# Kernel tuning notes

Hardware: AMD Instinct MI355X
Metric: run time of the kernel (lower is better)

The kernel has to match this reference:

```python
import jax, jax.numpy as jnp
import numpy as np

D_MODEL, D_K, D_V, N_HEADS, D_FF = 1024, 64, 64, 16, 2736
EPS_NORM = 1e-12   # F.normalize eps
EPS_RMS = 1e-6     # RMSNorm eps


def _rmsnorm(x, g):
    return x * jax.lax.rsqrt(jnp.mean(x * x, axis=-1, keepdims=True) + EPS_RMS) * g


def _l2norm(x):
    n = jnp.sqrt(jnp.sum(x * x, axis=-1, keepdims=True))
    return x / jnp.maximum(n, EPS_NORM)


def setup_inputs() -> dict:
    key = jax.random.key(0)
    ks = jax.random.split(key, 10)
    B, T = 2, 1024
    s_in = 0.1 / np.sqrt(D_MODEL)   # xavier-like small init, gain 0.1
    s_ff = 0.1 / np.sqrt(D_FF)
    return {
        "x": jax.random.normal(ks[0], (B, T, D_MODEL), jnp.float32),
        "Wq": jax.random.normal(ks[1], (D_MODEL, N_HEADS * D_K), jnp.float32) * s_in,
        "Wk": jax.random.normal(ks[2], (D_MODEL, N_HEADS * D_K), jnp.float32) * s_in,
        "Wv": jax.random.normal(ks[3], (D_MODEL, N_HEADS * D_V), jnp.float32) * s_in,
        "Wg": jax.random.normal(ks[4], (D_MODEL, N_HEADS * D_K), jnp.float32) * s_in,
        "Wo": jax.random.normal(ks[5], (N_HEADS * D_V, D_MODEL), jnp.float32) * s_in,
        "w1": jax.random.normal(ks[6], (D_MODEL, D_FF), jnp.float32) * s_in,
        "w2": jax.random.normal(ks[7], (D_MODEL, D_FF), jnp.float32) * s_in,
        "w3": jax.random.normal(ks[8], (D_FF, D_MODEL), jnp.float32) * s_ff,
        "g_attn": jnp.ones((D_MODEL,), jnp.float32),
        "g_ffn": jnp.ones((D_MODEL,), jnp.float32),
    }


def _gla(h, Wq, Wk, Wv, Wg, Wo):
    B, T, _ = h.shape
    q = _l2norm((h @ Wq).reshape(B, T, N_HEADS, D_K))
    k = _l2norm((h @ Wk).reshape(B, T, N_HEADS, D_K))
    v = (h @ Wv).reshape(B, T, N_HEADS, D_V)
    alpha = jax.nn.sigmoid(h @ Wg).reshape(B, T, N_HEADS, D_K)

    def step(S, inp):
        a_t, k_t, v_t, q_t = inp                       # [B,H,dk],[B,H,dk],[B,H,dv],[B,H,dk]
        S = a_t[..., None] * S + k_t[..., None] * v_t[..., None, :]   # [B,H,dk,dv]
        o_t = jnp.einsum('bhkv,bhk->bhv', S, q_t)
        return S, o_t

    S0 = jnp.zeros((B, N_HEADS, D_K, D_V), h.dtype)
    xs = (jnp.swapaxes(alpha, 0, 1), jnp.swapaxes(k, 0, 1),
          jnp.swapaxes(v, 0, 1), jnp.swapaxes(q, 0, 1))  # time-major [T,B,H,*]
    _, o = jax.lax.scan(step, S0, xs)                    # o: [T,B,H,dv]
    o = jnp.swapaxes(o, 0, 1).reshape(B, T, N_HEADS * D_V)
    return o @ Wo


def reference(x, Wq, Wk, Wv, Wg, Wo, w1, w2, w3, g_attn, g_ffn):
    # Pre-LN GLA block: x -> Norm -> GLA -> +res -> Norm -> SwiGLU -> +res
    h = _rmsnorm(x, g_attn)
    x = x + _gla(h, Wq, Wk, Wv, Wg, Wo)
    h = _rmsnorm(x, g_ffn)
    ffn = (jax.nn.silu(h @ w1) * (h @ w2)) @ w3
    return x + ffn
```

## Files before the change

### kernel.cpp

```cpp
#include <hip/hip_runtime.h>

typedef unsigned short ushort_t;
typedef unsigned int uint32;
typedef short short8 __attribute__((ext_vector_type(8)));
typedef float f32x4 __attribute__((ext_vector_type(4)));

#define MROWS 2048
#define DMODEL 1024
#define NH 16
#define DFF 2736
#define DFFP 2752
#define NBH 32

__device__ __forceinline__ float b2f(ushort_t u) {
  return __builtin_bit_cast(float, ((uint32)u) << 16);
}
__device__ __forceinline__ ushort_t f2b(float f) {
  uint32 u = __builtin_bit_cast(uint32, f);
  return (ushort_t)((u + 0x7FFFu + ((u >> 16) & 1u)) >> 16);
}
__device__ __forceinline__ float san(float v) {
  uint32 u = __builtin_bit_cast(uint32, v);
  return (((u >> 23) & 0xFFu) == 0xFFu) ? 0.0f : v;
}
__device__ __forceinline__ float sclamp(float v, float lim) {
  return fminf(fmaxf(san(v), -lim), lim);
}

typedef const __attribute__((address_space(1))) unsigned int* gas_ptr;
typedef __attribute__((address_space(3))) unsigned int* las_ptr;
__device__ __forceinline__ void gl_lds16(const void* g, void* l) {
  __builtin_amdgcn_global_load_lds((gas_ptr)g, (las_ptr)l, 16, 0, 0);
}

__device__ __forceinline__ void rmsnorm_body(
    const float* __restrict__ x, const float* __restrict__ g,
    ushort_t* __restrict__ out, int row, int tid) {
  size_t base = (size_t)row * DMODEL;
  int c0 = tid * 4;
  float4 t = *(const float4*)(x + base + c0);
  float v[4] = {t.x, t.y, t.z, t.w};
  float s = v[0]*v[0] + v[1]*v[1] + v[2]*v[2] + v[3]*v[3];
  for (int off = 32; off > 0; off >>= 1) s += __shfl_xor(s, off);
  __shared__ float red[4];
  int wave = tid >> 6, lane = tid & 63;
  if (lane == 0) red[wave] = s;
  __syncthreads();
  if (tid == 0) {
    float tt = red[0] + red[1] + red[2] + red[3];
    red[0] = rsqrtf(tt * (1.0f / DMODEL) + 1e-6f);
  }
  __syncthreads();
  float sc = red[0];
  float4 gg = *(const float4*)(g + c0);
  float gv[4] = {gg.x, gg.y, gg.z, gg.w};
  for (int j = 0; j < 4; ++j)
    out[base + c0 + j] = f2b(sclamp(v[j] * sc * gv[j], 1e4f));
}

__global__ __launch_bounds__(256) void rmsnorm_kernel(
    const float* __restrict__ x, const float* __restrict__ g,
    ushort_t* __restrict__ out) {
  rmsnorm_body(x, g, out, blockIdx.x, threadIdx.x);
}

__device__ __forceinline__ void transpose_tile(
    const float* __restrict__ src, ushort_t* __restrict__ d,
    int K, int N, int Kpad, int n0, int k0, int tid) {
  __shared__ ushort_t tile[32][33];
  int tx = tid & 31, ty = tid >> 5;
  #pragma unroll
  for (int i = 0; i < 4; ++i) {
    int k = k0 + ty + i * 8, n = n0 + tx;
    float v = (k < K && n < N) ? src[(size_t)k * N + n] : 0.0f;
    tile[ty + i * 8][tx] = f2b(v);
  }
  __syncthreads();
  #pragma unroll
  for (int i = 0; i < 4; ++i) {
    int r = ty + i * 8;
    d[(size_t)(n0 + r) * Kpad + k0 + tx] = tile[tx][r];
  }
}

__global__ __launch_bounds__(256) void transpose_kernel(
    const float* __restrict__ S0, const float* __restrict__ S1,
    const float* __restrict__ S2, const float* __restrict__ S3,
    ushort_t* __restrict__ dst, int K, int N, int Kpad, int Npad) {
  const float* src = (blockIdx.z == 0) ? S0 : (blockIdx.z == 1) ? S1
                   : (blockIdx.z == 2) ? S2 : S3;
  ushort_t* d = dst + (size_t)blockIdx.z * Npad * Kpad;
  transpose_tile(src, d, K, N, Kpad, blockIdx.x * 32, blockIdx.y * 32,
                 threadIdx.x);
}

__global__ __launch_bounds__(256) void transpose5_kernel(
    const float* __restrict__ S0, const float* __restrict__ S1,
    const float* __restrict__ S2, const float* __restrict__ S3,
    const float* __restrict__ S4,
    ushort_t* __restrict__ dA, ushort_t* __restrict__ dB) {
  int z = blockIdx.z;
  const float* src = (z == 0) ? S0 : (z == 1) ? S1 : (z == 2) ? S2
                   : (z == 3) ? S3 : S4;
  ushort_t* d = (z < 4) ? (dA + (size_t)z * 1024 * 1024) : dB;
  transpose_tile(src, d, 1024, 1024, 1024, blockIdx.x * 32, blockIdx.y * 32,
                 threadIdx.x);
}

__global__ __launch_bounds__(256) void transpose_ffn_kernel(
    const float* __restrict__ w1, const float* __restrict__ w2,
    const float* __restrict__ w3,
    ushort_t* __restrict__ dW12, ushort_t* __restrict__ dW3) {
  int z = blockIdx.z;
  const float* src; ushort_t* d; int K, N, Kpad, Npad;
  if (z < 2) {
    src = z ? w2 : w1; d = dW12 + (size_t)z * DFFP * 1024;
    K = 1024; N = DFF; Kpad = 1024; Npad = DFFP;
  } else {
    src = w3; d = dW3;
    K = DFF; N = 1024; Kpad = DFFP; Npad = 1024;
  }
  int n0 = blockIdx.x * 32, k0 = blockIdx.y * 32;
  if (n0 >= Npad || k0 >= Kpad) return;
  transpose_tile(src, d, K, N, Kpad, n0, k0, threadIdx.x);
}

__global__ __launch_bounds__(256) void setup_kernel(
    const float* __restrict__ x, const float* __restrict__ gat,
    ushort_t* __restrict__ h1,
    const float* __restrict__ Wq, const float* __restrict__ Wk,
    const float* __restrict__ Wv, const float* __restrict__ Wg,
    const float* __restrict__ Wo,
    ushort_t* __restrict__ dQKVG, ushort_t* __restrict__ dWo,
    const float* __restrict__ w1, const float* __restrict__ w2,
    const float* __restrict__ w3,
    ushort_t* __restrict__ dW12, ushort_t* __restrict__ dW3) {
  int bid = blockIdx.x, tid = threadIdx.x;
  if (bid < 2048) {
    rmsnorm_body(x, gat, h1, bid, tid);
  } else if (bid < 7168) {
    int idx = bid - 2048;
    int z = idx >> 10, rem = idx & 1023;
    const float* src = (z == 0) ? Wq : (z == 1) ? Wk : (z == 2) ? Wv
                     : (z == 3) ? Wg : Wo;
    ushort_t* d = (z < 4) ? (dQKVG + (size_t)z * 1024 * 1024) : dWo;
    transpose_tile(src, d, 1024, 1024, 1024, (rem & 31) * 32, (rem >> 5) * 32,
                   tid);
  } else {
    int fidx = bid - 7168;
    const float* src; ushort_t* d; int K, N, Kpad, bx, by;
    if (fidx < 5504) {
      int z = fidx / 2752, t = fidx % 2752;
      src = z ? w2 : w1; d = dW12 + (size_t)z * DFFP * 1024;
      K = 1024; N = DFF; Kpad = 1024;
      bx = t % 86; by = t / 86;
    } else {
      int t2 = fidx - 5504;
      src = w3; d = dW3;
      K = DFF; N = 1024; Kpad = DFFP;
      bx = t2 % 32; by = t2 / 32;
    }
    transpose_tile(src, d, K, N, Kpad, bx * 32, by * 32, tid);
  }
}

template<int MODE, int BM, int BN, int NB, int MINB>
__global__ __launch_bounds__(256, MINB) void gemm_kernel(
    const ushort_t* __restrict__ A, int lda,
    const ushort_t* __restrict__ Bt, int ldb, size_t boff, int K,
    float* __restrict__ outf, ushort_t* __restrict__ outb, int ldc,
    const float* __restrict__ resf) {
  constexpr int WM = BM / 2, WN = BN / 2;
  constexpr int MF = WM / 16, FN = WN / 16;
  __shared__ __align__(16) ushort_t As0[BM * 64];
  __shared__ __align__(16) ushort_t As1[BM * 64];
  __shared__ __align__(16) ushort_t Bs0[NB][BN * 64];
  __shared__ __align__(16) ushort_t Bs1[NB][BN * 64];
  int tid = threadIdx.x;
  int wave = tid >> 6, lane = tid & 63;
  int nwg = gridDim.x * gridDim.y;
  int orig = blockIdx.y * gridDim.x + blockIdx.x;
  int swz = (orig & 7) * (nwg >> 3) + (orig >> 3);
  int n0 = (swz / gridDim.y) * BN, m0 = (swz % gridDim.y) * BM;
  int wm = (wave >> 1) * WM, wn = (wave & 1) * WN;
  int arow = lane >> 3;
  int scol = (((lane & 7) ^ arow) & 7) * 8;
  int fm = lane & 15, fk = (lane >> 4) * 8;
  int xsw = (fm & 7) * 8;
  f32x4 zero = {0.f, 0.f, 0.f, 0.f};
  f32x4 acc[MF][FN];
  f32x4 acc2[NB == 2 ? MF : 1][NB == 2 ? FN : 1];
  #pragma unroll
  for (int i = 0; i < MF; ++i)
    #pragma unroll
    for (int j = 0; j < FN; ++j) {
      acc[i][j] = zero;
      if (NB == 2) acc2[i][j] = zero;
    }
  int nK = K >> 6;
  auto stage = [&](ushort_t (&Ad)[BM * 64], ushort_t (&Bd)[NB][BN * 64],
                   int kt) {
    int k0 = kt << 6;
    #pragma unroll
    for (int i = 0; i < BM / 32; ++i) {
      int g = i * 4 + wave;
      gl_lds16(A + (size_t)(m0 + g * 8 + arow) * lda + k0 + scol, &Ad[g * 512]);
    }
    #pragma unroll
    for (int nb = 0; nb < NB; ++nb)
      #pragma unroll
      for (int i = 0; i < BN / 32; ++i) {
        int g = i * 4 + wave;
        gl_lds16(Bt + nb * boff + (size_t)(n0 + g * 8 + arow) * ldb + k0 + scol,
                 &Bd[nb][g * 512]);
      }
  };
  auto compute = [&](const ushort_t (&Ad)[BM * 64],
                     const ushort_t (&Bd)[NB][BN * 64]) {
    #pragma unroll
    for (int kk = 0; kk < 64; kk += 32) {
      short8 a[MF];
      #pragma unroll
      for (int fi = 0; fi < MF; ++fi)
        a[fi] = *(const short8*)
            &Ad[(wm + fi * 16 + fm) * 64 + ((kk + fk) ^ xsw)];
      #pragma unroll
      for (int fj = 0; fj < FN; ++fj) {
        short8 b = *(const short8*)
            &Bd[0][(wn + fj * 16 + fm) * 64 + ((kk + fk) ^ xsw)];
        #pragma unroll
        for (int fi = 0; fi < MF; ++fi)
          acc[fi][fj] =
              __builtin_amdgcn_mfma_f32_16x16x32_bf16(a[fi], b, acc[fi][fj], 0, 0, 0);
        if (NB == 2) {
          short8 b2 = *(const short8*)
              &Bd[1][(wn + fj * 16 + fm) * 64 + ((kk + fk) ^ xsw)];
          #pragma unroll
          for (int fi = 0; fi < MF; ++fi)
            acc2[fi][fj] =
                __builtin_amdgcn_mfma_f32_16x16x32_bf16(a[fi], b2, acc2[fi][fj], 0, 0, 0);
        }
      }
    }
  };
  stage(As0, Bs0, 0);
  __syncthreads();
  int t = 0;
  for (;;) {
    if (t + 1 < nK) stage(As1, Bs1, t + 1);
    compute(As0, Bs0);
    __syncthreads();
    if (++t == nK) break;
    if (t + 1 < nK) stage(As0, Bs0, t + 1);
    compute(As1, Bs1);
    __syncthreads();
    if (++t == nK) break;
  }
  int rbase = m0 + wm + ((lane >> 4) << 2);
  #pragma unroll
  for (int fi = 0; fi < MF; ++fi)
    #pragma unroll
    for (int fj = 0; fj < FN; ++fj) {
      int col = n0 + wn + fj * 16 + fm;
      #pragma unroll
      for (int reg = 0; reg < 4; ++reg) {
        int row = rbase + fi * 16 + reg;
        float v = acc[fi][fj][reg];
        size_t oidx = (size_t)row * ldc + col;
        if (MODE == 0) {
          outb[oidx] = f2b(sclamp(v, 1e4f));
        } else if (MODE == 1) {
          outf[oidx] = sclamp(v, 0.25f) + resf[oidx];
        } else if (MODE == 2) {
          float y2 = sclamp(acc2[fi][fj][reg], 1e4f);
          float vc = fminf(fmaxf(san(v), -30.f), 30.f);
          float sg = vc / (1.0f + __expf(-vc));
          outb[oidx] = f2b(sclamp(sg * y2, 1e4f));
        } else {
          outf[oidx] = sclamp(v, 0.6f) + resf[oidx];
        }
      }
    }
}

template<int MODE>
__global__ __launch_bounds__(256) void gemm64_kernel(
    const ushort_t* __restrict__ A, int lda,
    const float* __restrict__ Bq, const float* __restrict__ Bk,
    const float* __restrict__ Bv, const float* __restrict__ Bg,
    int ldb, int K, int Nb,
    float* __restrict__ outf, ushort_t* __restrict__ outb, int ldc,
    const float* __restrict__ resf) {
  constexpr int NB = (MODE == 2) ? 2 : 1;
  __shared__ __align__(16) ushort_t As[64][72];
  __shared__ __align__(16) ushort_t Bs[NB][64][72];
  int tid = threadIdx.x;
  int wave = tid >> 6, lane = tid & 63;
  int m0 = blockIdx.y * 64;
  int n0 = blockIdx.x * 64;
  const float* B = Bq;
  int bcol = n0;
  f32x4 zero = {0.f, 0.f, 0.f, 0.f};
  f32x4 acc[4];
  f32x4 acc2[NB == 2 ? 4 : 1];
  for (int i = 0; i < 4; ++i) acc[i] = zero;
  if (NB == 2) for (int i = 0; i < 4; ++i) acc2[i] = zero;
  int r  = tid >> 2;
  int cb = (tid & 3) << 4;
  int fm = lane & 15;
  int fk = (lane >> 4) << 3;
  int nK = (K + 63) >> 6;
  for (int kt = 0; kt < nK; ++kt) {
    int k0 = kt << 6;
    for (int cc = 0; cc < 16; cc += 8) {
      int c = cb + cc;
      short8 val = {0,0,0,0,0,0,0,0};
      if (k0 + c + 8 <= K)
        val = *(const short8*)(A + (size_t)(m0 + r) * lda + k0 + c);
      *(short8*)&As[r][c] = val;
    }
    for (int nb = 0; nb < NB; ++nb) {
      const float* Bp = (nb == 0) ? B : Bk;
      for (int cc = 0; cc < 16; cc += 8) {
        int c = cb + cc;
        ushort_t val[8] = {0,0,0,0,0,0,0,0};
        if (k0 + r < K && bcol + c + 8 <= Nb) {
          const float* src = Bp + (size_t)(k0 + r) * ldb + bcol + c;
          float4 f0 = *(const float4*)(src);
          float4 f1 = *(const float4*)(src + 4);
          val[0] = f2b(f0.x); val[1] = f2b(f0.y);
          val[2] = f2b(f0.z); val[3] = f2b(f0.w);
          val[4] = f2b(f1.x); val[5] = f2b(f1.y);
          val[6] = f2b(f1.z); val[7] = f2b(f1.w);
        }
        for (int j = 0; j < 8; ++j) Bs[nb][c + j][r] = val[j];
      }
    }
    __syncthreads();
    for (int kk = 0; kk < 64; kk += 32) {
      short8 a = *(const short8*)&As[wave * 16 + fm][kk + fk];
      for (int nt = 0; nt < 4; ++nt) {
        short8 b = *(const short8*)&Bs[0][nt * 16 + fm][kk + fk];
        acc[nt] = __builtin_amdgcn_mfma_f32_16x16x32_bf16(a, b, acc[nt], 0, 0, 0);
        if (NB == 2) {
          short8 b2 = *(const short8*)&Bs[1][nt * 16 + fm][kk + fk];
          acc2[nt] = __builtin_amdgcn_mfma_f32_16x16x32_bf16(a, b2, acc2[nt], 0, 0, 0);
        }
      }
    }
    __syncthreads();
  }
  int rbase = m0 + wave * 16 + ((lane >> 4) << 2);
  for (int nt = 0; nt < 4; ++nt) {
    int col = n0 + nt * 16 + (lane & 15);
    for (int reg = 0; reg < 4; ++reg) {
      int row = rbase + reg;
      float v = acc[nt][reg];
      size_t oidx = (size_t)row * ldc + col;
      if (MODE == 2) {
        if (col < Nb) {
          float y2 = sclamp(acc2[nt][reg], 1e4f);
          float vc = fminf(fmaxf(san(v), -30.f), 30.f);
          float sg = vc / (1.0f + __expf(-vc));
          outb[oidx] = f2b(sclamp(sg * y2, 1e4f));
        }
      } else if (MODE == 3) {
        outf[oidx] = sclamp(v, 0.6f) + resf[oidx];
      }
    }
  }
}

__global__ __launch_bounds__(256) void prep_kernel(ushort_t* __restrict__ yq,
                                                   float* __restrict__ Bc) {
  int h = blockIdx.x, g = blockIdx.y;
  int bh = (g >> 4) * NH + h;
  int c = g & 15;
  int r0 = g * 64;
  int tid = threadIdx.x, wave = tid >> 6, lane = tid & 63;
  __shared__ float qs[64][65], ks[64][65], gs[64][65];
  for (int t = wave; t < 64; t += 4) {
    size_t rb = (size_t)(r0 + t) * 4096 + h * 64 + lane;
    float q = san(b2f(yq[rb]));
    float s = q * q;
    for (int off = 32; off > 0; off >>= 1) s += __shfl_xor(s, off);
    qs[t][lane] = q / fmaxf(sqrtf(s), 1e-12f);
    float k = san(b2f(yq[rb + 1024]));
    s = k * k;
    for (int off = 32; off > 0; off >>= 1) s += __shfl_xor(s, off);
    ks[t][lane] = k / fmaxf(sqrtf(s), 1e-12f);
    float a = fminf(fmaxf(san(b2f(yq[rb + 3072])), -30.f), 30.f);
    gs[t][lane] = 1.0f / (1.0f + __expf(-a));
  }
  __syncthreads();
  for (int j = 0; j < 16; ++j) {
    int kd = wave * 16 + j;
    float b = gs[lane][kd];
    #pragma unroll
    for (int off = 1; off < 64; off <<= 1) {
      float p = __shfl_up(b, off);
      if (lane >= off) b *= p;
    }
    b = fmaxf(b, 1e-28f);
    float inv = fminf(1.0f / b, 1e26f);
    qs[lane][kd] = sclamp(qs[lane][kd] * b, 1e30f);
    ks[lane][kd] = sclamp(ks[lane][kd] * inv, 1e30f);
    if (lane == 63) Bc[((size_t)bh * 16 + c) * 64 + kd] = b;
  }
  __syncthreads();
  for (int t = wave; t < 64; t += 4) {
    size_t rb = (size_t)(r0 + t) * 4096 + h * 64 + lane;
    yq[rb] = f2b(qs[t][lane]);
    yq[rb + 1024] = f2b(ks[t][lane]);
  }
}

__global__ __launch_bounds__(256) void prep_ktv_kernel(
    ushort_t* __restrict__ yq, float* __restrict__ Bc,
    float* __restrict__ KtV) {
  int h = blockIdx.x, g = blockIdx.y;
  int bh = (g >> 4) * NH + h;
  int c = g & 15;
  int r0 = g * 64;
  int tid = threadIdx.x, wave = tid >> 6, lane = tid & 63;
  __shared__ float qs[64][65], ks[64][65], gs[64][65];
  __shared__ ushort_t Kt[64][72];
  __shared__ ushort_t Vt[64][72];
  for (int t = wave; t < 64; t += 4) {
    size_t rb = (size_t)(r0 + t) * 4096 + h * 64 + lane;
    float q = san(b2f(yq[rb]));
    float s = q * q;
    for (int off = 32; off > 0; off >>= 1) s += __shfl_xor(s, off);
    qs[t][lane] = q / fmaxf(sqrtf(s), 1e-12f);
    float k = san(b2f(yq[rb + 1024]));
    s = k * k;
    for (int off = 32; off > 0; off >>= 1) s += __shfl_xor(s, off);
    ks[t][lane] = k / fmaxf(sqrtf(s), 1e-12f);
    float a = fminf(fmaxf(san(b2f(yq[rb + 3072])), -30.f), 30.f);
    gs[t][lane] = 1.0f / (1.0f + __expf(-a));
  }
  for (int i = tid; i < 512; i += 256) {
    int t = i >> 3, v8 = (i & 7) * 8;
    short8 v8v = *(const short8*)(yq + (size_t)(r0 + t) * 4096 + 2048 +
                                  h * 64 + v8);
    #pragma unroll
    for (int j = 0; j < 8; ++j) Vt[v8 + j][t] = (ushort_t)v8v[j];
  }
  __syncthreads();
  for (int j = 0; j < 16; ++j) {
    int kd = wave * 16 + j;
    float b = gs[lane][kd];
    #pragma unroll
    for (int off = 1; off < 64; off <<= 1) {
      float p = __shfl_up(b, off);
      if (lane >= off) b *= p;
    }
    b = fmaxf(b, 1e-28f);
    float inv = fminf(1.0f / b, 1e26f);
    qs[lane][kd] = sclamp(qs[lane][kd] * b, 1e30f);
    ks[lane][kd] = sclamp(ks[lane][kd] * inv, 1e30f);
    if (lane == 63) Bc[((size_t)bh * 16 + c) * 64 + kd] = b;
  }
  __syncthreads();
  for (int t = wave; t < 64; t += 4) {
    size_t rb = (size_t)(r0 + t) * 4096 + h * 64 + lane;
    yq[rb] = f2b(qs[t][lane]);
    ushort_t kb = f2b(ks[t][lane]);
    yq[rb + 1024] = kb;
    Kt[lane][t] = kb;
  }
  __syncthreads();
  int wm = wave * 16;
  int fm = lane & 15, fk = (lane >> 4) * 8;
  f32x4 zero = {0.f, 0.f, 0.f, 0.f};
  f32x4 acc[4] = {zero, zero, zero, zero};
  #pragma unroll
  for (int kk = 0; kk < 64; kk += 32) {
    short8 a = *(const short8*)&Kt[wm + fm][kk + fk];
    #pragma unroll
    for (int f = 0; f < 4; ++f) {
      short8 b = *(const short8*)&Vt[f * 16 + fm][kk + fk];
      acc[f] = __builtin_amdgcn_mfma_f32_16x16x32_bf16(a, b, acc[f], 0, 0, 0);
    }
  }
  size_t obase = (((size_t)bh * 16 + c) * 64) * 64;
  int krow = wm + ((lane >> 4) << 2);
  #pragma unroll
  for (int f = 0; f < 4; ++f) {
    int v = f * 16 + fm;
    #pragma unroll
    for (int reg = 0; reg < 4; ++reg)
      KtV[obase + (size_t)(krow + reg) * 64 + v] = acc[f][reg];
  }
}

__global__ __launch_bounds__(256) void scan_kernel(
    const float* __restrict__ KtV, const float* __restrict__ Bc,
    float* __restrict__ Sbuf) {
  int q = blockIdx.x, bh = blockIdx.y;
  int tid = threadIdx.x;
  int v4 = tid & 15, kloc = tid >> 4;
  int k = q * 16 + kloc;
  float4 S = {0.f, 0.f, 0.f, 0.f};
  size_t base = ((size_t)bh * 16) * 4096 + (size_t)k * 64 + v4 * 4;
  #pragma unroll
  for (int c = 0; c < 16; ++c) {
    size_t a = base + (size_t)c * 4096;
    *(float4*)(Sbuf + a) = S;
    float4 kv = *(const float4*)(KtV + a);
    float bc = Bc[((size_t)bh * 16 + c) * 64 + k];
    S.x = sclamp((S.x + kv.x) * bc, 1e6f);
    S.y = sclamp((S.y + kv.y) * bc, 1e6f);
    S.z = sclamp((S.z + kv.z) * bc, 1e6f);
    S.w = sclamp((S.w + kv.w) * bc, 1e6f);
  }
}

__global__ __launch_bounds__(256) void state_kernel(
    const ushort_t* __restrict__ yq, const float* __restrict__ Bc,
    float* __restrict__ Sbuf) {
  int vs = blockIdx.x;
  int bh = blockIdx.y;
  int bidx = bh >> 4, h = bh & 15;
  int tid = threadIdx.x;
  int k = tid & 63, v4 = tid >> 6;
  __shared__ float kbs[64][64];
  __shared__ float vls[64][16];
  float S[4] = {0.f, 0.f, 0.f, 0.f};
  for (int c = 0; c < 16; ++c) {
    size_t sb = (((size_t)bh * 16 + c) * 64 + k) * 64 + vs * 16 + v4 * 4;
    float4 st; st.x = S[0]; st.y = S[1]; st.z = S[2]; st.w = S[3];
    *(float4*)(Sbuf + sb) = st;
    int r0 = bidx * 1024 + c * 64;
    for (int i = tid; i < 4096; i += 256) {
      int t = i >> 6, kk = i & 63;
      kbs[t][kk] = b2f(yq[(size_t)(r0 + t) * 4096 + 1024 + h * 64 + kk]);
    }
    for (int i = tid; i < 1024; i += 256) {
      int t = i >> 4, vv = i & 15;
      vls[t][vv] = b2f(yq[(size_t)(r0 + t) * 4096 + 2048 + h * 64 + vs * 16 + vv]);
    }
    __syncthreads();
    for (int t = 0; t < 64; ++t) {
      float kv = kbs[t][k];
      S[0] += kv * vls[t][v4 * 4 + 0];
      S[1] += kv * vls[t][v4 * 4 + 1];
      S[2] += kv * vls[t][v4 * 4 + 2];
      S[3] += kv * vls[t][v4 * 4 + 3];
    }
    float bc = Bc[((size_t)bh * 16 + c) * 64 + k];
    S[0] = sclamp(S[0] * bc, 1e6f); S[1] = sclamp(S[1] * bc, 1e6f);
    S[2] = sclamp(S[2] * bc, 1e6f); S[3] = sclamp(S[3] * bc, 1e6f);
    __syncthreads();
  }
}

__global__ __launch_bounds__(256) void outk_kernel(
    const ushort_t* __restrict__ yq, const float* __restrict__ Sbuf,
    ushort_t* __restrict__ o) {
  int h = blockIdx.x;
  int g = blockIdx.y;
  int bh = (g >> 4) * NH + h;
  int c = g & 15;
  int r0 = g * 64;
  int tid = threadIdx.x, wave = tid >> 6, lane = tid & 63;
  __shared__ ushort_t Qs[64][72];
  __shared__ ushort_t Kbs[64][72];
  __shared__ ushort_t Vt[64][72];
  __shared__ ushort_t St[64][72];
  __shared__ ushort_t Ps[64][72];
  for (int i = tid; i < 512; i += 256) {
    int t = i >> 3, k8 = (i & 7) * 8;
    size_t rb = (size_t)(r0 + t) * 4096 + h * 64 + k8;
    *(short8*)&Qs[t][k8]  = *(const short8*)(yq + rb);
    *(short8*)&Kbs[t][k8] = *(const short8*)(yq + rb + 1024);
    short8 v8 = *(const short8*)(yq + rb + 2048);
    #pragma unroll
    for (int j = 0; j < 8; ++j) Vt[k8 + j][t] = (ushort_t)v8[j];
  }
  size_t sbase = (((size_t)bh * 16 + c) * 64) * 64;
  for (int i = tid; i < 1024; i += 256) {
    int kd = i >> 4, v4 = (i & 15) * 4;
    float4 s4 = *(const float4*)(Sbuf + sbase + (size_t)kd * 64 + v4);
    St[v4 + 0][kd] = f2b(sclamp(s4.x, 1e6f));
    St[v4 + 1][kd] = f2b(sclamp(s4.y, 1e6f));
    St[v4 + 2][kd] = f2b(sclamp(s4.z, 1e6f));
    St[v4 + 3][kd] = f2b(sclamp(s4.w, 1e6f));
  }
  __syncthreads();
  int wm = wave * 16;
  int fm = lane & 15, fk = (lane >> 4) * 8;
  f32x4 zero = {0.f, 0.f, 0.f, 0.f};
  f32x4 oacc[4] = {zero, zero, zero, zero};
  f32x4 pacc[4] = {zero, zero, zero, zero};
  #pragma unroll
  for (int kk = 0; kk < 64; kk += 32) {
    short8 a = *(const short8*)&Qs[wm + fm][kk + fk];
    #pragma unroll
    for (int f = 0; f < 4; ++f) {
      short8 bS = *(const short8*)&St[f * 16 + fm][kk + fk];
      oacc[f] = __builtin_amdgcn_mfma_f32_16x16x32_bf16(a, bS, oacc[f], 0, 0, 0);
      short8 bK = *(const short8*)&Kbs[f * 16 + fm][kk + fk];
      pacc[f] = __builtin_amdgcn_mfma_f32_16x16x32_bf16(a, bK, pacc[f], 0, 0, 0);
    }
  }
  int prow = wm + ((lane >> 4) << 2);
  #pragma unroll
  for (int f = 0; f < 4; ++f) {
    int s = f * 16 + fm;
    #pragma unroll
    for (int reg = 0; reg < 4; ++reg) {
      float pv = (s <= prow + reg) ? pacc[f][reg] : 0.0f;
      Ps[prow + reg][s] = f2b(pv);
    }
  }
  __syncthreads();
  #pragma unroll
  for (int kk = 0; kk < 64; kk += 32) {
    short8 a = *(const short8*)&Ps[wm + fm][kk + fk];
    #pragma unroll
    for (int f = 0; f < 4; ++f) {
      short8 bV = *(const short8*)&Vt[f * 16 + fm][kk + fk];
      oacc[f] = __builtin_amdgcn_mfma_f32_16x16x32_bf16(a, bV, oacc[f], 0, 0, 0);
    }
  }
  #pragma unroll
  for (int f = 0; f < 4; ++f) {
    int v = f * 16 + fm;
    #pragma unroll
    for (int reg = 0; reg < 4; ++reg) {
      int row = prow + reg;
      o[(size_t)(r0 + row) * 1024 + h * 64 + v] = f2b(sclamp(oacc[f][reg], 100.f));
    }
  }
}

__global__ void sentinel_kernel(float* __restrict__ out, int env) {
  if (threadIdx.x == 0 && blockIdx.x == 0)
    out[0] = 1.0e6f + 1000.0f * (float)env;
}

extern "C" void kernel_launch(void* const* d_in, const int* in_sizes, int n_in,
                              void* d_out, int out_size, void* d_ws, size_t ws_size,
                              hipStream_t stream) {
  const float* x    = (const float*)d_in[0];
  const float* Wq   = (const float*)d_in[1];
  const float* Wk   = (const float*)d_in[2];
  const float* Wv   = (const float*)d_in[3];
  const float* Wg   = (const float*)d_in[4];
  const float* Wo   = (const float*)d_in[5];
  const float* w1   = (const float*)d_in[6];
  const float* w2   = (const float*)d_in[7];
  const float* w3   = (const float*)d_in[8];
  const float* gat  = (const float*)d_in[9];
  const float* gff  = (const float*)d_in[10];
  float* out = (float*)d_out;

  char* ws = (char*)d_ws;
  const size_t R0o = 0;
  const size_t R1o = (size_t)16 * 1024 * 1024;
  const size_t R2o = (size_t)20 * 1024 * 1024;
  const size_t R3o = R2o + 128 * 1024;
  const size_t R4o = R3o + (size_t)8 * 1024 * 1024;
  const size_t W12B = (size_t)2 * DFFP * 1024 * 2;
  const size_t W3B  = (size_t)1024 * DFFP * 2;
  const size_t R5o  = R4o + (size_t)16 * 1024 * 1024;
  const size_t NEED_SMALL = R4o + 4096;
  const size_t NEED_BIG   = R4o + W12B + 4096;
  const size_t NEED_BIG2  = R5o + W12B + W3B + 4096;

  ushort_t* yq     = (ushort_t*)(ws + R0o);
  ushort_t* ff     = (ushort_t*)(ws + R0o);
  ushort_t* h1     = (ushort_t*)(ws + R1o);
  ushort_t* obuf   = (ushort_t*)(ws + R1o);
  ushort_t* h2     = (ushort_t*)(ws + R1o);
  float*    Bc     = (float*)   (ws + R2o);
  ushort_t* BtQKVG = (ushort_t*)(ws + R3o);
  float*    Sbuf   = (float*)   (ws + R3o);
  float*    x2     = (float*)   (ws + R3o);
  float*    KtV    = (float*)   (ws + R4o);

  int env = 0;
  if (ws_size < NEED_SMALL) env |= 1;
  if (n_in != 11) env |= 2;
  if (in_sizes[0] != 2097152) env |= 4;
  if (n_in == 11 && (in_sizes[1] != 1048576 || in_sizes[6] != 1024 * 2736 ||
                     in_sizes[8] != 2736 * 1024 || in_sizes[9] != 1024)) env |= 8;
  if (out_size != 2097152) env |= 16;
  if (env) {
    sentinel_kernel<<<1, 64, 0, stream>>>(out, env);
    return;
  }
  bool big  = (ws_size >= NEED_BIG);
  bool big2 = (ws_size >= NEED_BIG2);
  ushort_t* BtWo = big ? (ushort_t*)(ws + R4o + (size_t)8 * 1024 * 1024)
                       : (ushort_t*)(ws + R0o);
  ushort_t* BtW12 = big2 ? (ushort_t*)(ws + R5o)
                         : (ushort_t*)(ws + R4o);
  ushort_t* BtW3  = big2 ? (ushort_t*)(ws + R5o + W12B)
                         : (ushort_t*)(ws + R4o);

  if (big2) {
    setup_kernel<<<15424, 256, 0, stream>>>(
        x, gat, h1, Wq, Wk, Wv, Wg, Wo, BtQKVG, BtWo, w1, w2, w3, BtW12, BtW3);
  } else {
    rmsnorm_kernel<<<MROWS, 256, 0, stream>>>(x, gat, h1);
    if (big) {
      transpose5_kernel<<<dim3(32, 32, 5), 256, 0, stream>>>(
          Wq, Wk, Wv, Wg, Wo, BtQKVG, BtWo);
    } else {
      transpose_kernel<<<dim3(32, 32, 4), 256, 0, stream>>>(
          Wq, Wk, Wv, Wg, BtQKVG, 1024, 1024, 1024, 1024);
    }
  }
  gemm_kernel<0, 128, 128, 1, 2><<<dim3(32, 16), 256, 0, stream>>>(
      h1, DMODEL, BtQKVG, DMODEL, 0, DMODEL, nullptr, yq, 4096, nullptr);
  if (big) {
    prep_ktv_kernel<<<dim3(16, 32), 256, 0, stream>>>(yq, Bc, KtV);
    scan_kernel<<<dim3(4, 32), 256, 0, stream>>>(KtV, Bc, Sbuf);
  } else {
    prep_kernel<<<dim3(16, 32), 256, 0, stream>>>(yq, Bc);
    state_kernel<<<dim3(4, 32), 256, 0, stream>>>(yq, Bc, Sbuf);
  }
  outk_kernel<<<dim3(16, 32), 256, 0, stream>>>(yq, Sbuf, obuf);
  if (!big)
    transpose_kernel<<<dim3(32, 32, 1), 256, 0, stream>>>(
        Wo, nullptr, nullptr, nullptr, BtWo, 1024, 1024, 1024, 1024);
  gemm_kernel<1, 32, 64, 1, 5><<<dim3(16, 64), 256, 0, stream>>>(
      obuf, DMODEL, BtWo, DMODEL, 0, DMODEL, x2, nullptr, DMODEL, x);
  rmsnorm_kernel<<<MROWS, 256, 0, stream>>>(x2, gff, h2);
  if (big2) {
    gemm_kernel<2, 128, 64, 2, 2><<<dim3(43, 16), 256, 0, stream>>>(
        h2, DMODEL, BtW12, DMODEL, (size_t)DFFP * 1024, DMODEL,
        nullptr, ff, DFFP, nullptr);
    gemm_kernel<3, 32, 64, 1, 5><<<dim3(16, 64), 256, 0, stream>>>(
        ff, DFFP, BtW3, DFFP, 0, DFFP, out, nullptr, DMODEL, x2);
  } else {
    gemm64_kernel<2><<<dim3(43, 32), 256, 0, stream>>>(
        h2, DMODEL, w1, w2, nullptr, nullptr, DFF, DMODEL, DFF,
        nullptr, ff, DFF, nullptr);
    gemm64_kernel<3><<<dim3(16, 32), 256, 0, stream>>>(
        ff, DFF, w3, nullptr, nullptr, nullptr, DMODEL, DFF, DMODEL,
        out, nullptr, DMODEL, x2);
  }
}
```

Baseline: 256.8 us.

## Add triple-buffered direct-to-LDS GEMM for residual projections; store chunk states in bf16

Adds a new GEMM kernel with a three-stage LDS ring fed by direct global-to-LDS loads. It uses explicit vmcnt waits, an XOR-swizzled layout and a swizzled block order, and replaces the Wo and w3 projection GEMMs. The chunk state buffer is now written as bf16 by the scan/state kernels and read directly by outk, which halves its traffic and drops the conversion in outk. The deeper pipeline uses more LDS per block. The unused FFN transpose kernel is removed, and the W12/W3 pointers now always assume the large workspace.

```diff
diff --git a/kernel.cpp b/kernel.cpp
--- a/kernel.cpp
+++ b/kernel.cpp
@@ -3,6 +3,7 @@
 typedef unsigned short ushort_t;
 typedef unsigned int uint32;
 typedef short short8 __attribute__((ext_vector_type(8)));
+typedef unsigned short ushort4v __attribute__((ext_vector_type(4)));
 typedef float f32x4 __attribute__((ext_vector_type(4)));
 
 #define MROWS 2048
@@ -105,24 +106,6 @@
   ushort_t* d = (z < 4) ? (dA + (size_t)z * 1024 * 1024) : dB;
   transpose_tile(src, d, 1024, 1024, 1024, blockIdx.x * 32, blockIdx.y * 32,
                  threadIdx.x);
-}
-
-__global__ __launch_bounds__(256) void transpose_ffn_kernel(
-    const float* __restrict__ w1, const float* __restrict__ w2,
-    const float* __restrict__ w3,
-    ushort_t* __restrict__ dW12, ushort_t* __restrict__ dW3) {
-  int z = blockIdx.z;
-  const float* src; ushort_t* d; int K, N, Kpad, Npad;
-  if (z < 2) {
-    src = z ? w2 : w1; d = dW12 + (size_t)z * DFFP * 1024;
-    K = 1024; N = DFF; Kpad = 1024; Npad = DFFP;
-  } else {
-    src = w3; d = dW3;
-    K = DFF; N = 1024; Kpad = DFFP; Npad = 1024;
-  }
-  int n0 = blockIdx.x * 32, k0 = blockIdx.y * 32;
-  if (n0 >= Npad || k0 >= Kpad) return;
-  transpose_tile(src, d, K, N, Kpad, n0, k0, threadIdx.x);
 }
 
 __global__ __launch_bounds__(256) void setup_kernel(
@@ -279,6 +262,112 @@
         } else {
           outf[oidx] = sclamp(v, 0.6f) + resf[oidx];
         }
+      }
+    }
+}
+
+template<int MODE, int BM, int BN, int MINB>
+__global__ __launch_bounds__(256, MINB) void gemm_p3_kernel(
+    const ushort_t* __restrict__ A, int lda,
+    const ushort_t* __restrict__ Bt, int ldb, int K,
+    float* __restrict__ outf, int ldc, const float* __restrict__ resf) {
+  constexpr int WM = BM / 2, WN = BN / 2;
+  constexpr int MF = WM / 16, FN = WN / 16;
+  constexpr int L = BM / 32 + BN / 32;
+  __shared__ __align__(16) ushort_t A0[BM * 64];
+  __shared__ __align__(16) ushort_t A1[BM * 64];
+  __shared__ __align__(16) ushort_t A2[BM * 64];
+  __shared__ __align__(16) ushort_t B0[BN * 64];
+  __shared__ __align__(16) ushort_t B1[BN * 64];
+  __shared__ __align__(16) ushort_t B2[BN * 64];
+  int tid = threadIdx.x;
+  int wave = tid >> 6, lane = tid & 63;
+  int nwg = gridDim.x * gridDim.y;
+  int orig = blockIdx.y * gridDim.x + blockIdx.x;
+  int swz = (orig & 7) * (nwg >> 3) + (orig >> 3);
+  int n0 = (swz / gridDim.y) * BN, m0 = (swz % gridDim.y) * BM;
+  int wm = (wave >> 1) * WM, wn = (wave & 1) * WN;
+  int arow = lane >> 3;
+  int scol = (((lane & 7) ^ arow) & 7) * 8;
+  int fm = lane & 15, fk = (lane >> 4) * 8;
+  int xsw = (fm & 7) * 8;
+  f32x4 zero = {0.f, 0.f, 0.f, 0.f};
+  f32x4 acc[MF][FN];
+  #pragma unroll
+  for (int i = 0; i < MF; ++i)
+    #pragma unroll
+    for (int j = 0; j < FN; ++j) acc[i][j] = zero;
+  int nK = K >> 6;
+  auto stage = [&](ushort_t (&Ad)[BM * 64], ushort_t (&Bd)[BN * 64], int kt) {
+    int k0 = kt << 6;
+    #pragma unroll
+    for (int i = 0; i < BM / 32; ++i) {
+      int g = i * 4 + wave;
+      gl_lds16(A + (size_t)(m0 + g * 8 + arow) * lda + k0 + scol, &Ad[g * 512]);
+    }
+    #pragma unroll
+    for (int i = 0; i < BN / 32; ++i) {
+      int g = i * 4 + wave;
+      gl_lds16(Bt + (size_t)(n0 + g * 8 + arow) * ldb + k0 + scol, &Bd[g * 512]);
+    }
+  };
+  auto compute = [&](const ushort_t (&Ad)[BM * 64],
+                     const ushort_t (&Bd)[BN * 64]) {
+    #pragma unroll
+    for (int kk = 0; kk < 64; kk += 32) {
+      short8 a[MF];
+      #pragma unroll
+      for (int fi = 0; fi < MF; ++fi)
+        a[fi] = *(const short8*)
+            &Ad[(wm + fi * 16 + fm) * 64 + ((kk + fk) ^ xsw)];
+      #pragma unroll
+      for (int fj = 0; fj < FN; ++fj) {
+        short8 b = *(const short8*)
+            &Bd[(wn + fj * 16 + fm) * 64 + ((kk + fk) ^ xsw)];
+        #pragma unroll
+        for (int fi = 0; fi < MF; ++fi)
+          acc[fi][fj] =
+              __builtin_amdgcn_mfma_f32_16x16x32_bf16(a[fi], b, acc[fi][fj], 0, 0, 0);
+      }
+    }
+  };
+  auto wait_cnt = [&](int t) {
+    if (t + 1 < nK) asm volatile("s_waitcnt vmcnt(%0)" :: "n"(L) : "memory");
+    else            asm volatile("s_waitcnt vmcnt(0)" ::: "memory");
+  };
+  stage(A0, B0, 0);
+  if (nK > 1) stage(A1, B1, 1);
+  int t = 0;
+  for (;;) {
+    wait_cnt(t);
+    __builtin_amdgcn_s_barrier();
+    if (t + 2 < nK) stage(A2, B2, t + 2);
+    compute(A0, B0);
+    if (++t == nK) break;
+    wait_cnt(t);
+    __builtin_amdgcn_s_barrier();
+    if (t + 2 < nK) stage(A0, B0, t + 2);
+    compute(A1, B1);
+    if (++t == nK) break;
+    wait_cnt(t);
+    __builtin_amdgcn_s_barrier();
+    if (t + 2 < nK) stage(A1, B1, t + 2);
+    compute(A2, B2);
+    if (++t == nK) break;
+  }
+  int rbase = m0 + wm + ((lane >> 4) << 2);
+  #pragma unroll
+  for (int fi = 0; fi < MF; ++fi)
+    #pragma unroll
+    for (int fj = 0; fj < FN; ++fj) {
+      int col = n0 + wn + fj * 16 + fm;
+      #pragma unroll
+      for (int reg = 0; reg < 4; ++reg) {
+        int row = rbase + fi * 16 + reg;
+        float v = acc[fi][fj][reg];
+        size_t oidx = (size_t)row * ldc + col;
+        if (MODE == 1) outf[oidx] = sclamp(v, 0.25f) + resf[oidx];
+        else           outf[oidx] = sclamp(v, 0.6f) + resf[oidx];
       }
     }
 }
@@ -496,7 +585,7 @@
 
 __global__ __launch_bounds__(256) void scan_kernel(
     const float* __restrict__ KtV, const float* __restrict__ Bc,
-    float* __restrict__ Sbuf) {
+    ushort_t* __restrict__ Sbuf) {
   int q = blockIdx.x, bh = blockIdx.y;
   int tid = threadIdx.x;
   int v4 = tid & 15, kloc = tid >> 4;
@@ -506,7 +595,9 @@
   #pragma unroll
   for (int c = 0; c < 16; ++c) {
     size_t a = base + (size_t)c * 4096;
-    *(float4*)(Sbuf + a) = S;
+    ushort4v sb = {f2b(sclamp(S.x, 1e6f)), f2b(sclamp(S.y, 1e6f)),
+                   f2b(sclamp(S.z, 1e6f)), f2b(sclamp(S.w, 1e6f))};
+    *(ushort4v*)(Sbuf + a) = sb;
     float4 kv = *(const float4*)(KtV + a);
     float bc = Bc[((size_t)bh * 16 + c) * 64 + k];
     S.x = sclamp((S.x + kv.x) * bc, 1e6f);
@@ -518,7 +609,7 @@
 
 __global__ __launch_bounds__(256) void state_kernel(
     const ushort_t* __restrict__ yq, const float* __restrict__ Bc,
-    float* __restrict__ Sbuf) {
+    ushort_t* __restrict__ Sbuf) {
   int vs = blockIdx.x;
   int bh = blockIdx.y;
   int bidx = bh >> 4, h = bh & 15;
@@ -529,8 +620,9 @@
   float S[4] = {0.f, 0.f, 0.f, 0.f};
   for (int c = 0; c < 16; ++c) {
     size_t sb = (((size_t)bh * 16 + c) * 64 + k) * 64 + vs * 16 + v4 * 4;
-    float4 st; st.x = S[0]; st.y = S[1]; st.z = S[2]; st.w = S[3];
-    *(float4*)(Sbuf + sb) = st;
+    ushort4v st = {f2b(sclamp(S[0], 1e6f)), f2b(sclamp(S[1], 1e6f)),
+                   f2b(sclamp(S[2], 1e6f)), f2b(sclamp(S[3], 1e6f))};
+    *(ushort4v*)(Sbuf + sb) = st;
     int r0 = bidx * 1024 + c * 64;
     for (int i = tid; i < 4096; i += 256) {
       int t = i >> 6, kk = i & 63;
@@ -556,7 +648,7 @@
 }
 
 __global__ __launch_bounds__(256) void outk_kernel(
-    const ushort_t* __restrict__ yq, const float* __restrict__ Sbuf,
+    const ushort_t* __restrict__ yq, const ushort_t* __restrict__ Sbuf,
     ushort_t* __restrict__ o) {
   int h = blockIdx.x;
   int g = blockIdx.y;
@@ -581,11 +673,11 @@
   size_t sbase = (((size_t)bh * 16 + c) * 64) * 64;
   for (int i = tid; i < 1024; i += 256) {
     int kd = i >> 4, v4 = (i & 15) * 4;
-    float4 s4 = *(const float4*)(Sbuf + sbase + (size_t)kd * 64 + v4);
-    St[v4 + 0][kd] = f2b(sclamp(s4.x, 1e6f));
-    St[v4 + 1][kd] = f2b(sclamp(s4.y, 1e6f));
-    St[v4 + 2][kd] = f2b(sclamp(s4.z, 1e6f));
-    St[v4 + 3][kd] = f2b(sclamp(s4.w, 1e6f));
+    ushort4v s4 = *(const ushort4v*)(Sbuf + sbase + (size_t)kd * 64 + v4);
+    St[v4 + 0][kd] = s4.x;
+    St[v4 + 1][kd] = s4.y;
+    St[v4 + 2][kd] = s4.z;
+    St[v4 + 3][kd] = s4.w;
   }
   __syncthreads();
   int wm = wave * 16;
@@ -676,7 +768,7 @@
   ushort_t* h2     = (ushort_t*)(ws + R1o);
   float*    Bc     = (float*)   (ws + R2o);
   ushort_t* BtQKVG = (ushort_t*)(ws + R3o);
-  float*    Sbuf   = (float*)   (ws + R3o);
+  ushort_t* Sbuf   = (ushort_t*)(ws + R3o);
   float*    x2     = (float*)   (ws + R3o);
   float*    KtV    = (float*)   (ws + R4o);
 
@@ -695,10 +787,8 @@
   bool big2 = (ws_size >= NEED_BIG2);
   ushort_t* BtWo = big ? (ushort_t*)(ws + R4o + (size_t)8 * 1024 * 1024)
                        : (ushort_t*)(ws + R0o);
-  ushort_t* BtW12 = big2 ? (ushort_t*)(ws + R5o)
-                         : (ushort_t*)(ws + R4o);
-  ushort_t* BtW3  = big2 ? (ushort_t*)(ws + R5o + W12B)
-                         : (ushort_t*)(ws + R4o);
+  ushort_t* BtW12 = (ushort_t*)(ws + R5o);
+  ushort_t* BtW3  = (ushort_t*)(ws + R5o + W12B);
 
   if (big2) {
     setup_kernel<<<15424, 256, 0, stream>>>(
@@ -726,15 +816,15 @@
   if (!big)
     transpose_kernel<<<dim3(32, 32, 1), 256, 0, stream>>>(
         Wo, nullptr, nullptr, nullptr, BtWo, 1024, 1024, 1024, 1024);
-  gemm_kernel<1, 32, 64, 1, 5><<<dim3(16, 64), 256, 0, stream>>>(
-      obuf, DMODEL, BtWo, DMODEL, 0, DMODEL, x2, nullptr, DMODEL, x);
+  gemm_p3_kernel<1, 32, 64, 4><<<dim3(16, 64), 256, 0, stream>>>(
+      obuf, DMODEL, BtWo, DMODEL, DMODEL, x2, DMODEL, x);
   rmsnorm_kernel<<<MROWS, 256, 0, stream>>>(x2, gff, h2);
   if (big2) {
     gemm_kernel<2, 128, 64, 2, 2><<<dim3(43, 16), 256, 0, stream>>>(
         h2, DMODEL, BtW12, DMODEL, (size_t)DFFP * 1024, DMODEL,
         nullptr, ff, DFFP, nullptr);
-    gemm_kernel<3, 32, 64, 1, 5><<<dim3(16, 64), 256, 0, stream>>>(
-        ff, DFFP, BtW3, DFFP, 0, DFFP, out, nullptr, DMODEL, x2);
+    gemm_p3_kernel<3, 32, 64, 4><<<dim3(16, 64), 256, 0, stream>>>(
+        ff, DFFP, BtW3, DFFP, DFFP, out, DMODEL, x2);
   } else {
     gemm64_kernel<2><<<dim3(43, 32), 256, 0, stream>>>(
         h2, DMODEL, w1, w2, nullptr, nullptr, DFF, DMODEL, DFF,
```

Result: no change. 257.2 us (+0.2%).
